# Performance work log

Measured on AMD Instinct MI355X. Metric: run time of the kernel, lower is better.

Reference implementation:

```python
import jax, jax.numpy as jnp
import numpy as np

B, C, CI, H, W = 8, 256, 128, 48, 48


def conv1x1(x, w, b):
    # x: (B,C,H,W), w: (CI,C), b: (CI,)
    return jnp.einsum('bchw,oc->bohw', x, w) + b[None, :, None, None]


def setup_inputs() -> dict:
    key = jax.random.key(0)
    ks = jax.random.split(key, 14)
    s = 1.0 / np.sqrt(C)
    d = {
        'x_1': jax.random.normal(ks[0], (B, C, H, W), jnp.float32),
        'x_2': jax.random.normal(ks[1], (B, C, H, W), jnp.float32),
    }
    names = ['v1', 'k1', 'q1', 'v2', 'k2', 'q2']
    for i, n in enumerate(names):
        d['w_' + n] = jax.random.uniform(ks[2 + 2 * i], (CI, C), jnp.float32, -s, s)
        d['b_' + n] = jax.random.uniform(ks[3 + 2 * i], (CI,), jnp.float32, -s, s)
    return d


def reference(x_1, x_2, w_v1, b_v1, w_k1, b_k1, w_q1, b_q1,
              w_v2, b_v2, w_k2, b_k2, w_q2, b_q2):
    b, ci, h, w = x_1.shape[0], w_v1.shape[0], x_1.shape[2], x_1.shape[3]
    n = h * w
    V1 = conv1x1(x_1, w_v1, b_v1).reshape(b, ci, n)
    K1 = conv1x1(x_1, w_k1, b_k1).reshape(b, ci, n)
    Q1 = conv1x1(x_1, w_q1, b_q1).reshape(b, ci, n)
    V2 = conv1x1(x_2, w_v2, b_v2).reshape(b, ci, n)
    K2 = conv1x1(x_2, w_k2, b_k2).reshape(b, ci, n)
    Q2 = conv1x1(x_2, w_q2, b_q2).reshape(b, ci, n)
    # sigmoid-gated cross attention, (B, N, N)
    R12 = jax.nn.sigmoid(jnp.einsum('bcn,bcm->bnm', Q1, K2))
    R21 = jax.nn.sigmoid(jnp.einsum('bcn,bcm->bnm', Q2, K1))
    Fu1 = jnp.einsum('bnm,bcm->bcn', R12, V2).reshape(b, ci, h, w)
    Fu2 = jnp.einsum('bnm,bcm->bcn', R21, V1).reshape(b, ci, h, w)
    y_1 = jnp.concatenate([x_1, Fu1], axis=1)
    y_2 = jnp.concatenate([x_2, Fu2], axis=1)
    return (y_1, y_2)
```

## Files before the change

### kernel.cpp

```cpp
#include <hip/hip_runtime.h>
#include <hip/hip_bf16.h>


typedef __bf16 bf16;
typedef __bf16 bf16x8 __attribute__((ext_vector_type(8)));
typedef __bf16 bf16x4 __attribute__((ext_vector_type(4)));
typedef float f32x4 __attribute__((ext_vector_type(4)));
typedef float f32x16 __attribute__((ext_vector_type(16)));
typedef unsigned int u32x4 __attribute__((ext_vector_type(4)));

#define NB 8
#define NC 256
#define NCI 128
#define NHW 2304
#define NT32 72

__global__ __launch_bounds__(256) void wconv_kernel(
    const float* __restrict__ w0, const float* __restrict__ w1,
    const float* __restrict__ w2, const float* __restrict__ w3,
    const float* __restrict__ w4, const float* __restrict__ w5,
    bf16* __restrict__ dst)
{
    int idx = (blockIdx.x * 256 + threadIdx.x) * 8;
    int m = idx >> 15;
    int off = idx & 32767;
    const float* w = (m == 0) ? w0 : (m == 1) ? w1 : (m == 2) ? w2
                   : (m == 3) ? w3 : (m == 4) ? w4 : w5;
    f32x4 a0 = *(const f32x4*)(w + off);
    f32x4 a1 = *(const f32x4*)(w + off + 4);
    bf16x8 o;
    #pragma unroll
    for (int j = 0; j < 4; ++j) { o[j] = (bf16)a0[j]; o[4 + j] = (bf16)a1[j]; }
    *(bf16x8*)(dst + idx) = o;
}

__global__ __launch_bounds__(256) void qkv_kernel(
    const float* __restrict__ x1, const float* __restrict__ x2,
    const bf16* __restrict__ wb,
    const float* __restrict__ bv1, const float* __restrict__ bk1, const float* __restrict__ bq1,
    const float* __restrict__ bv2, const float* __restrict__ bk2, const float* __restrict__ bq2,
    bf16* __restrict__ Qt, bf16* __restrict__ Kt, bf16* __restrict__ Vt,
    float* __restrict__ out)
{
    __shared__ __align__(16) bf16 Xt[32 * 264];

    int gid = blockIdx.x;
    int nt = gid % NT32;
    int s = (gid / NT32) & 1;
    int b = gid / (2 * NT32);
    int n0 = nt * 32;

    const float* x = s ? x2 : x1;
    const bf16* wv = wb + (size_t)(s * 3 + 0) * (NCI * NC);
    const bf16* wk = wb + (size_t)(s * 3 + 1) * (NCI * NC);
    const bf16* wq = wb + (size_t)(s * 3 + 2) * (NCI * NC);
    const float* bv = s ? bv2 : bv1;
    const float* bk = s ? bk2 : bk1;
    const float* bq = s ? bq2 : bq1;
    float* outy = out + (size_t)s * (NB * 384 * NHW);

    int tid = threadIdx.x;
    {
        int n_off = (tid & 3) * 8;
        int c0l = tid >> 2;
        #pragma unroll
        for (int i = 0; i < 4; ++i) {
            int c = c0l + i * 64;
            const float* src = x + ((size_t)(b * NC + c) * NHW + n0 + n_off);
            f32x4 a0 = *(const f32x4*)src;
            f32x4 a1 = *(const f32x4*)(src + 4);
            float* dsty = outy + ((size_t)(b * 384 + c) * NHW + n0 + n_off);
            *(f32x4*)dsty = a0;
            *(f32x4*)(dsty + 4) = a1;
            #pragma unroll
            for (int j = 0; j < 4; ++j) {
                Xt[(n_off + j) * 264 + c] = (bf16)a0[j];
                Xt[(n_off + 4 + j) * 264 + c] = (bf16)a1[j];
            }
        }
    }
    __syncthreads();

    int lane = tid & 63;
    int wid = tid >> 6;
    int row = lane & 15, quad = lane >> 4;
    int ci_base = wid * 32;

    f32x4 acc[3][2][2];
    #pragma unroll
    for (int t = 0; t < 3; ++t)
        #pragma unroll
        for (int mi = 0; mi < 2; ++mi)
            #pragma unroll
            for (int j = 0; j < 2; ++j)
                acc[t][mi][j] = (f32x4){0.f, 0.f, 0.f, 0.f};

    const bf16* wptr[3] = {wq, wk, wv};
    #pragma unroll
    for (int ks = 0; ks < 8; ++ks) {
        int c0 = ks * 32 + quad * 8;
        bf16x8 bfrag[2];
        #pragma unroll
        for (int j = 0; j < 2; ++j)
            bfrag[j] = *(const bf16x8*)&Xt[(j * 16 + row) * 264 + c0];
        #pragma unroll
        for (int t = 0; t < 3; ++t) {
            #pragma unroll
            for (int mi = 0; mi < 2; ++mi) {
                bf16x8 afrag = *(const bf16x8*)&wptr[t][(size_t)(ci_base + mi * 16 + row) * NC + c0];
                #pragma unroll
                for (int j = 0; j < 2; ++j)
                    acc[t][mi][j] = __builtin_amdgcn_mfma_f32_16x16x32_bf16(
                        afrag, bfrag[j], acc[t][mi][j], 0, 0, 0);
            }
        }
    }

    size_t qkbase = ((size_t)s * NB + b) * NHW * NCI;
    size_t vbase  = ((size_t)s * NB + b) * NCI * NHW;
    #pragma unroll
    for (int mi = 0; mi < 2; ++mi) {
        int ci0 = ci_base + mi * 16 + quad * 4;
        f32x4 bq4 = *(const f32x4*)&bq[ci0];
        f32x4 bk4 = *(const f32x4*)&bk[ci0];
        f32x4 bv4 = *(const f32x4*)&bv[ci0];
        #pragma unroll
        for (int j = 0; j < 2; ++j) {
            int n = n0 + j * 16 + row;
            bf16x4 pk;
            #pragma unroll
            for (int r = 0; r < 4; ++r) pk[r] = (bf16)(acc[0][mi][j][r] + bq4[r]);
            *(bf16x4*)&Qt[qkbase + (size_t)n * NCI + ci0] = pk;
            #pragma unroll
            for (int r = 0; r < 4; ++r) pk[r] = (bf16)(acc[1][mi][j][r] + bk4[r]);
            *(bf16x4*)&Kt[qkbase + (size_t)n * NCI + ci0] = pk;
            #pragma unroll
            for (int r = 0; r < 4; ++r)
                Vt[vbase + (size_t)(ci0 + r) * NHW + n] = (bf16)(acc[2][mi][j][r] + bv4[r]);
        }
    }
}

__global__ __launch_bounds__(256, 2) void attn_kernel(
    const bf16* __restrict__ Qt, const bf16* __restrict__ Kt, const bf16* __restrict__ Vt,
    float* __restrict__ out)
{
    __shared__ __align__(16) bf16 KH[2 * 64 * 128];
    __shared__ __align__(16) bf16 VH[2 * 128 * 64];

    int gid = blockIdx.x;
    int pair = (gid & 7) * 2 + ((gid >> 3) & 1);
    int nb = gid >> 4;
    int dir = pair & 1;
    int b = pair >> 1;

    int tid = threadIdx.x;
    int lane = tid & 63;
    int w = tid >> 6;
    int ns = w & 1;
    int mh = w >> 1;
    int col = lane & 31;
    int hi = lane >> 5;

    int sq = dir, skv = dir ^ 1;
    const bf16* q = Qt + ((size_t)sq  * NB + b) * (NHW * NCI);
    const bf16* k = Kt + ((size_t)skv * NB + b) * (NHW * NCI);
    const bf16* v = Vt + ((size_t)skv * NB + b) * (NCI * NHW);
    float* outy = out + (size_t)dir * (NB * 384 * NHW) + ((size_t)b * 384 + 256) * NHW;

    int kgoff[4], vgoff[4], kloff[4], vloff[4];
    #pragma unroll
    for (int i = 0; i < 4; ++i) {
        int c = tid + i * 256;
        int kr = c >> 4, kc = c & 15;
        kgoff[i] = kr * NCI + kc * 8;
        kloff[i] = kr * 128 + ((kc ^ (kr & 15)) * 8);
        int vr = c >> 3, vc = c & 7;
        vgoff[i] = vr * NHW + vc * 8;
        vloff[i] = vr * 64 + ((vc ^ (vr & 7)) * 8);
    }

    int nw = nb * 64 + ns * 32;
    bf16x8 qf[8];
    #pragma unroll
    for (int kq = 0; kq < 8; ++kq)
        qf[kq] = *(const bf16x8*)&q[(size_t)(nw + col) * NCI + kq * 16 + hi * 8];

    f32x16 o0, o1, o2, o3;
    #pragma unroll
    for (int j = 0; j < 16; ++j) { o0[j] = 0.f; o1[j] = 0.f; o2[j] = 0.f; o3[j] = 0.f; }

    bf16x8 rk[2][4], rv[2][4];
    #pragma unroll
    for (int h = 0; h < 2; ++h) {
        const bf16* kp = k + (size_t)(h * 1152) * NCI;
        const bf16* vp = v + h * 1152;
        #pragma unroll
        for (int i = 0; i < 4; ++i) {
            rk[h][i] = *(const bf16x8*)(kp + kgoff[i]);
            rv[h][i] = *(const bf16x8*)(vp + vgoff[i]);
        }
    }

    const bf16* KB = &KH[mh * (64 * 128)];
    const bf16* VB = &VH[mh * (128 * 64)];

    for (int it = 0; it < 18; ++it) {
        __syncthreads();
        #pragma unroll
        for (int h = 0; h < 2; ++h)
            #pragma unroll
            for (int i = 0; i < 4; ++i) {
                *(bf16x8*)&KH[h * (64 * 128) + kloff[i]] = rk[h][i];
                *(bf16x8*)&VH[h * (128 * 64) + vloff[i]] = rv[h][i];
            }
        __syncthreads();
        if (it < 17) {
            #pragma unroll
            for (int h = 0; h < 2; ++h) {
                const bf16* kp = k + (size_t)(h * 1152 + (it + 1) * 64) * NCI;
                const bf16* vp = v + (h * 1152 + (it + 1) * 64);
                #pragma unroll
                for (int i = 0; i < 4; ++i) {
                    rk[h][i] = *(const bf16x8*)(kp + kgoff[i]);
                    rv[h][i] = *(const bf16x8*)(vp + vgoff[i]);
                }
            }
        }

        f32x16 s0, s1;
        #pragma unroll
        for (int j = 0; j < 16; ++j) { s0[j] = 0.f; s1[j] = 0.f; }

        __builtin_amdgcn_s_setprio(1);
        #pragma unroll
        for (int kq = 0; kq < 8; ++kq) {
            bf16x8 kf0 = *(const bf16x8*)&KB[col * 128 + (((2 * kq + hi) ^ (col & 15)) * 8)];
            s0 = __builtin_amdgcn_mfma_f32_32x32x16_bf16(kf0, qf[kq], s0, 0, 0, 0);
            bf16x8 kf1 = *(const bf16x8*)&KB[(32 + col) * 128 + (((2 * kq + hi) ^ (col & 15)) * 8)];
            s1 = __builtin_amdgcn_mfma_f32_32x32x16_bf16(kf1, qf[kq], s1, 0, 0, 0);
        }
        __builtin_amdgcn_s_setprio(0);

        u32x4 pbw[4];
        #pragma unroll
        for (int ms = 0; ms < 2; ++ms) {
            float p[16];
            #pragma unroll
            for (int r = 0; r < 16; ++r) {
                float sv = (ms == 0) ? s0[r] : s1[r];
                float e = __expf(-sv);
                p[r] = __builtin_amdgcn_rcpf(1.0f + e);
            }
            #pragma unroll
            for (int kst = 0; kst < 2; ++kst) {
                unsigned int a0, a1, b0, b1;
                asm("v_cvt_pk_bf16_f32 %0, %1, %2" : "=v"(a0) : "v"(p[8*kst+0]), "v"(p[8*kst+1]));
                asm("v_cvt_pk_bf16_f32 %0, %1, %2" : "=v"(a1) : "v"(p[8*kst+2]), "v"(p[8*kst+3]));
                asm("v_cvt_pk_bf16_f32 %0, %1, %2" : "=v"(b0) : "v"(p[8*kst+4]), "v"(p[8*kst+5]));
                asm("v_cvt_pk_bf16_f32 %0, %1, %2" : "=v"(b1) : "v"(p[8*kst+6]), "v"(p[8*kst+7]));
                asm volatile("v_permlane32_swap_b32 %0, %1" : "+v"(a0), "+v"(b0));
                asm volatile("v_permlane32_swap_b32 %0, %1" : "+v"(a1), "+v"(b1));
                pbw[ms * 2 + kst] = (u32x4){a0, a1, b0, b1};
            }
        }

        __builtin_amdgcn_s_setprio(1);
        #pragma unroll
        for (int km = 0; km < 4; ++km) {
            bf16x8 pf = __builtin_bit_cast(bf16x8, pbw[km]);
            {
                bf16x8 vf = *(const bf16x8*)&VB[(0 * 32 + col) * 64 + (((2 * km + hi) ^ (col & 7)) * 8)];
                o0 = __builtin_amdgcn_mfma_f32_32x32x16_bf16(vf, pf, o0, 0, 0, 0);
            }
            {
                bf16x8 vf = *(const bf16x8*)&VB[(1 * 32 + col) * 64 + (((2 * km + hi) ^ (col & 7)) * 8)];
                o1 = __builtin_amdgcn_mfma_f32_32x32x16_bf16(vf, pf, o1, 0, 0, 0);
            }
            {
                bf16x8 vf = *(const bf16x8*)&VB[(2 * 32 + col) * 64 + (((2 * km + hi) ^ (col & 7)) * 8)];
                o2 = __builtin_amdgcn_mfma_f32_32x32x16_bf16(vf, pf, o2, 0, 0, 0);
            }
            {
                bf16x8 vf = *(const bf16x8*)&VB[(3 * 32 + col) * 64 + (((2 * km + hi) ^ (col & 7)) * 8)];
                o3 = __builtin_amdgcn_mfma_f32_32x32x16_bf16(vf, pf, o3, 0, 0, 0);
            }
        }
        __builtin_amdgcn_s_setprio(0);
    }

    float* RED = (float*)KH;

    auto red_write = [&](float* buf, const f32x16 oa, const f32x16 ob) {
        #pragma unroll
        for (int g = 0; g < 4; ++g) {
            f32x4 va, vb;
            #pragma unroll
            for (int j = 0; j < 4; ++j) { va[j] = oa[g * 4 + j]; vb[j] = ob[g * 4 + j]; }
            *(f32x4*)&buf[lane * 32 + ((g ^ (lane & 7)) * 4)] = va;
            *(f32x4*)&buf[lane * 32 + (((4 + g) ^ (lane & 7)) * 4)] = vb;
        }
    };
    auto red_fin = [&](float* buf, f32x16& oa, f32x16& ob, int ctbase) {
        #pragma unroll
        for (int g = 0; g < 4; ++g) {
            f32x4 va = *(const f32x4*)&buf[lane * 32 + ((g ^ (lane & 7)) * 4)];
            f32x4 vb = *(const f32x4*)&buf[lane * 32 + (((4 + g) ^ (lane & 7)) * 4)];
            #pragma unroll
            for (int j = 0; j < 4; ++j) { oa[g * 4 + j] += va[j]; ob[g * 4 + j] += vb[j]; }
        }
        #pragma unroll
        for (int r = 0; r < 16; ++r) {
            int cr = (r & 3) + 8 * (r >> 2) + 4 * hi;
            outy[(size_t)(ctbase * 32 + cr) * NHW + nw + col] = oa[r];
            outy[(size_t)((ctbase + 1) * 32 + cr) * NHW + nw + col] = ob[r];
        }
    };

    __syncthreads();
    if (mh == 0) red_write(RED + (ns * 2 + 0) * 2048, o2, o3);
    else         red_write(RED + (ns * 2 + 1) * 2048, o0, o1);
    __syncthreads();
    if (mh == 0) red_fin(RED + (ns * 2 + 1) * 2048, o0, o1, 0);
    else         red_fin(RED + (ns * 2 + 0) * 2048, o2, o3, 2);
}

extern "C" void kernel_launch(void* const* d_in, const int* in_sizes, int n_in,
                              void* d_out, int out_size, void* d_ws, size_t ws_size,
                              hipStream_t stream) {
    const float* x1  = (const float*)d_in[0];
    const float* x2  = (const float*)d_in[1];
    const float* wv1 = (const float*)d_in[2];  const float* bv1 = (const float*)d_in[3];
    const float* wk1 = (const float*)d_in[4];  const float* bk1 = (const float*)d_in[5];
    const float* wq1 = (const float*)d_in[6];  const float* bq1 = (const float*)d_in[7];
    const float* wv2 = (const float*)d_in[8];  const float* bv2 = (const float*)d_in[9];
    const float* wk2 = (const float*)d_in[10]; const float* bk2 = (const float*)d_in[11];
    const float* wq2 = (const float*)d_in[12]; const float* bq2 = (const float*)d_in[13];
    float* out = (float*)d_out;

    size_t per = (size_t)2 * NB * NHW * NCI;
    bf16* Qt = (bf16*)d_ws;
    bf16* Kt = Qt + per;
    bf16* Vt = Kt + per;
    bf16* wb = Vt + per;

    wconv_kernel<<<dim3(96), dim3(256), 0, stream>>>(wv1, wk1, wq1, wv2, wk2, wq2, wb);

    qkv_kernel<<<dim3(NB * 2 * NT32), dim3(256), 0, stream>>>(
        x1, x2, wb, bv1, bk1, bq1, bv2, bk2, bq2, Qt, Kt, Vt, out);

    attn_kernel<<<dim3(NB * 2 * 36), dim3(256), 0, stream>>>(Qt, Kt, Vt, out);
}
```

Baseline: 234.9 us.

## Split attention KV sequence four ways across 8 waves with LDS-resident Q

```diff
diff --git a/kernel.cpp b/kernel.cpp
--- a/kernel.cpp
+++ b/kernel.cpp
@@ -141,12 +141,14 @@
     }
 }
 
-__global__ __launch_bounds__(256, 2) void attn_kernel(
+__global__ __launch_bounds__(512, 4) void attn_kernel(
     const bf16* __restrict__ Qt, const bf16* __restrict__ Kt, const bf16* __restrict__ Vt,
     float* __restrict__ out)
 {
-    __shared__ __align__(16) bf16 KH[2 * 64 * 128];
-    __shared__ __align__(16) bf16 VH[2 * 128 * 64];
+    __shared__ __align__(16) bf16 SMEM[40960];
+    bf16* KQ = SMEM;
+    bf16* VQ = SMEM + 16384;
+    bf16* QL = SMEM + 32768;
 
     int gid = blockIdx.x;
     int pair = (gid & 7) * 2 + ((gid >> 3) & 1);
@@ -158,7 +160,7 @@
     int lane = tid & 63;
     int w = tid >> 6;
     int ns = w & 1;
-    int mh = w >> 1;
+    int mq = w >> 1;
     int col = lane & 31;
     int hi = lane >> 5;
 
@@ -168,161 +170,171 @@
     const bf16* v = Vt + ((size_t)skv * NB + b) * (NCI * NHW);
     float* outy = out + (size_t)dir * (NB * 384 * NHW) + ((size_t)b * 384 + 256) * NHW;
 
+    #pragma unroll
+    for (int i = 0; i < 2; ++i) {
+        int c = tid + i * 512;
+        int qr = c >> 4, qc = c & 15;
+        bf16x8 t = *(const bf16x8*)&q[(size_t)(nb * 64 + qr) * NCI + qc * 8];
+        *(bf16x8*)&QL[qr * 128 + ((qc ^ (qr & 15)) * 8)] = t;
+    }
+
     int kgoff[4], vgoff[4], kloff[4], vloff[4];
     #pragma unroll
     for (int i = 0; i < 4; ++i) {
-        int c = tid + i * 256;
-        int kr = c >> 4, kc = c & 15;
-        kgoff[i] = kr * NCI + kc * 8;
-        kloff[i] = kr * 128 + ((kc ^ (kr & 15)) * 8);
-        int vr = c >> 3, vc = c & 7;
-        vgoff[i] = vr * NHW + vc * 8;
-        vloff[i] = vr * 64 + ((vc ^ (vr & 7)) * 8);
+        int c = tid + i * 512;
+        int qd = c >> 9, cc = c & 511;
+        int kr = cc >> 4, kc = cc & 15;
+        kgoff[i] = (qd * 576 + kr) * NCI + kc * 8;
+        kloff[i] = qd * 4096 + kr * 128 + ((kc ^ (kr & 15)) * 8);
+        int vr = cc >> 2, vc = cc & 3;
+        vgoff[i] = vr * NHW + qd * 576 + vc * 8;
+        vloff[i] = qd * 4096 + vr * 32 + ((vc ^ ((vr >> 1) & 3)) * 8);
     }
 
     int nw = nb * 64 + ns * 32;
-    bf16x8 qf[8];
-    #pragma unroll
-    for (int kq = 0; kq < 8; ++kq)
-        qf[kq] = *(const bf16x8*)&q[(size_t)(nw + col) * NCI + kq * 16 + hi * 8];
 
     f32x16 o0, o1, o2, o3;
     #pragma unroll
     for (int j = 0; j < 16; ++j) { o0[j] = 0.f; o1[j] = 0.f; o2[j] = 0.f; o3[j] = 0.f; }
 
-    bf16x8 rk[2][4], rv[2][4];
-    #pragma unroll
-    for (int h = 0; h < 2; ++h) {
-        const bf16* kp = k + (size_t)(h * 1152) * NCI;
-        const bf16* vp = v + h * 1152;
-        #pragma unroll
-        for (int i = 0; i < 4; ++i) {
-            rk[h][i] = *(const bf16x8*)(kp + kgoff[i]);
-            rv[h][i] = *(const bf16x8*)(vp + vgoff[i]);
-        }
-    }
-
-    const bf16* KB = &KH[mh * (64 * 128)];
-    const bf16* VB = &VH[mh * (128 * 64)];
+    bf16x8 rk[4], rv[4];
+    #pragma unroll
+    for (int i = 0; i < 4; ++i) {
+        rk[i] = *(const bf16x8*)(k + kgoff[i]);
+        rv[i] = *(const bf16x8*)(v + vgoff[i]);
+    }
+
+    int krd = mq * 4096 + col * 128;
+    int qrd = (ns * 32 + col) * 128;
+    int cswz = col & 15;
+    int vsw = (col >> 1) & 3;
+    int vrd = mq * 4096 + col * 32;
 
     for (int it = 0; it < 18; ++it) {
         __syncthreads();
         #pragma unroll
-        for (int h = 0; h < 2; ++h)
+        for (int i = 0; i < 4; ++i) {
+            *(bf16x8*)&KQ[kloff[i]] = rk[i];
+            *(bf16x8*)&VQ[vloff[i]] = rv[i];
+        }
+        __syncthreads();
+
+        f32x16 s;
+        #pragma unroll
+        for (int j = 0; j < 16; ++j) s[j] = 0.f;
+
+        __builtin_amdgcn_s_setprio(1);
+        #pragma unroll
+        for (int kq = 0; kq < 8; ++kq) {
+            int ch = ((2 * kq + hi) ^ cswz) * 8;
+            bf16x8 kf = *(const bf16x8*)&KQ[krd + ch];
+            bf16x8 qf = *(const bf16x8*)&QL[qrd + ch];
+            s = __builtin_amdgcn_mfma_f32_32x32x16_bf16(kf, qf, s, 0, 0, 0);
+        }
+        __builtin_amdgcn_s_setprio(0);
+
+        if (it < 17) {
+            size_t ko = (size_t)(it + 1) * 4096;
+            int vo = (it + 1) * 32;
             #pragma unroll
             for (int i = 0; i < 4; ++i) {
-                *(bf16x8*)&KH[h * (64 * 128) + kloff[i]] = rk[h][i];
-                *(bf16x8*)&VH[h * (128 * 64) + vloff[i]] = rv[h][i];
-            }
-        __syncthreads();
-        if (it < 17) {
-            #pragma unroll
-            for (int h = 0; h < 2; ++h) {
-                const bf16* kp = k + (size_t)(h * 1152 + (it + 1) * 64) * NCI;
-                const bf16* vp = v + (h * 1152 + (it + 1) * 64);
-                #pragma unroll
-                for (int i = 0; i < 4; ++i) {
-                    rk[h][i] = *(const bf16x8*)(kp + kgoff[i]);
-                    rv[h][i] = *(const bf16x8*)(vp + vgoff[i]);
-                }
-            }
-        }
-
-        f32x16 s0, s1;
-        #pragma unroll
-        for (int j = 0; j < 16; ++j) { s0[j] = 0.f; s1[j] = 0.f; }
+                rk[i] = *(const bf16x8*)(k + ko + kgoff[i]);
+                rv[i] = *(const bf16x8*)(v + vo + vgoff[i]);
+            }
+        }
+
+        float p[16];
+        #pragma unroll
+        for (int r = 0; r < 16; ++r) {
+            float e = __expf(-s[r]);
+            p[r] = __builtin_amdgcn_rcpf(1.0f + e);
+        }
+        u32x4 pbw[2];
+        #pragma unroll
+        for (int kst = 0; kst < 2; ++kst) {
+            unsigned int a0, a1, b0, b1;
+            asm("v_cvt_pk_bf16_f32 %0, %1, %2" : "=v"(a0) : "v"(p[8*kst+0]), "v"(p[8*kst+1]));
+            asm("v_cvt_pk_bf16_f32 %0, %1, %2" : "=v"(a1) : "v"(p[8*kst+2]), "v"(p[8*kst+3]));
+            asm("v_cvt_pk_bf16_f32 %0, %1, %2" : "=v"(b0) : "v"(p[8*kst+4]), "v"(p[8*kst+5]));
+            asm("v_cvt_pk_bf16_f32 %0, %1, %2" : "=v"(b1) : "v"(p[8*kst+6]), "v"(p[8*kst+7]));
+            asm volatile("v_permlane32_swap_b32 %0, %1" : "+v"(a0), "+v"(b0));
+            asm volatile("v_permlane32_swap_b32 %0, %1" : "+v"(a1), "+v"(b1));
+            pbw[kst] = (u32x4){a0, a1, b0, b1};
+        }
 
         __builtin_amdgcn_s_setprio(1);
         #pragma unroll
-        for (int kq = 0; kq < 8; ++kq) {
-            bf16x8 kf0 = *(const bf16x8*)&KB[col * 128 + (((2 * kq + hi) ^ (col & 15)) * 8)];
-            s0 = __builtin_amdgcn_mfma_f32_32x32x16_bf16(kf0, qf[kq], s0, 0, 0, 0);
-            bf16x8 kf1 = *(const bf16x8*)&KB[(32 + col) * 128 + (((2 * kq + hi) ^ (col & 15)) * 8)];
-            s1 = __builtin_amdgcn_mfma_f32_32x32x16_bf16(kf1, qf[kq], s1, 0, 0, 0);
+        for (int km = 0; km < 2; ++km) {
+            bf16x8 pf = __builtin_bit_cast(bf16x8, pbw[km]);
+            int mch = ((2 * km + hi) ^ vsw) * 8;
+            {
+                bf16x8 vf = *(const bf16x8*)&VQ[vrd + 0 * 1024 + mch];
+                o0 = __builtin_amdgcn_mfma_f32_32x32x16_bf16(vf, pf, o0, 0, 0, 0);
+            }
+            {
+                bf16x8 vf = *(const bf16x8*)&VQ[vrd + 1 * 1024 + mch];
+                o1 = __builtin_amdgcn_mfma_f32_32x32x16_bf16(vf, pf, o1, 0, 0, 0);
+            }
+            {
+                bf16x8 vf = *(const bf16x8*)&VQ[vrd + 2 * 1024 + mch];
+                o2 = __builtin_amdgcn_mfma_f32_32x32x16_bf16(vf, pf, o2, 0, 0, 0);
+            }
+            {
+                bf16x8 vf = *(const bf16x8*)&VQ[vrd + 3 * 1024 + mch];
+                o3 = __builtin_amdgcn_mfma_f32_32x32x16_bf16(vf, pf, o3, 0, 0, 0);
+            }
         }
         __builtin_amdgcn_s_setprio(0);
-
-        u32x4 pbw[4];
-        #pragma unroll
-        for (int ms = 0; ms < 2; ++ms) {
-            float p[16];
-            #pragma unroll
-            for (int r = 0; r < 16; ++r) {
-                float sv = (ms == 0) ? s0[r] : s1[r];
-                float e = __expf(-sv);
-                p[r] = __builtin_amdgcn_rcpf(1.0f + e);
-            }
-            #pragma unroll
-            for (int kst = 0; kst < 2; ++kst) {
-                unsigned int a0, a1, b0, b1;
-                asm("v_cvt_pk_bf16_f32 %0, %1, %2" : "=v"(a0) : "v"(p[8*kst+0]), "v"(p[8*kst+1]));
-                asm("v_cvt_pk_bf16_f32 %0, %1, %2" : "=v"(a1) : "v"(p[8*kst+2]), "v"(p[8*kst+3]));
-                asm("v_cvt_pk_bf16_f32 %0, %1, %2" : "=v"(b0) : "v"(p[8*kst+4]), "v"(p[8*kst+5]));
-                asm("v_cvt_pk_bf16_f32 %0, %1, %2" : "=v"(b1) : "v"(p[8*kst+6]), "v"(p[8*kst+7]));
-                asm volatile("v_permlane32_swap_b32 %0, %1" : "+v"(a0), "+v"(b0));
-                asm volatile("v_permlane32_swap_b32 %0, %1" : "+v"(a1), "+v"(b1));
-                pbw[ms * 2 + kst] = (u32x4){a0, a1, b0, b1};
-            }
-        }
-
-        __builtin_amdgcn_s_setprio(1);
-        #pragma unroll
-        for (int km = 0; km < 4; ++km) {
-            bf16x8 pf = __builtin_bit_cast(bf16x8, pbw[km]);
-            {
-                bf16x8 vf = *(const bf16x8*)&VB[(0 * 32 + col) * 64 + (((2 * km + hi) ^ (col & 7)) * 8)];
-                o0 = __builtin_amdgcn_mfma_f32_32x32x16_bf16(vf, pf, o0, 0, 0, 0);
-            }
-            {
-                bf16x8 vf = *(const bf16x8*)&VB[(1 * 32 + col) * 64 + (((2 * km + hi) ^ (col & 7)) * 8)];
-                o1 = __builtin_amdgcn_mfma_f32_32x32x16_bf16(vf, pf, o1, 0, 0, 0);
-            }
-            {
-                bf16x8 vf = *(const bf16x8*)&VB[(2 * 32 + col) * 64 + (((2 * km + hi) ^ (col & 7)) * 8)];
-                o2 = __builtin_amdgcn_mfma_f32_32x32x16_bf16(vf, pf, o2, 0, 0, 0);
-            }
-            {
-                bf16x8 vf = *(const bf16x8*)&VB[(3 * 32 + col) * 64 + (((2 * km + hi) ^ (col & 7)) * 8)];
-                o3 = __builtin_amdgcn_mfma_f32_32x32x16_bf16(vf, pf, o3, 0, 0, 0);
-            }
-        }
-        __builtin_amdgcn_s_setprio(0);
-    }
-
-    float* RED = (float*)KH;
-
-    auto red_write = [&](float* buf, const f32x16 oa, const f32x16 ob) {
+    }
+
+    float* RED = (float*)SMEM;
+
+    auto wpart = [&](float* buf, const f32x16& a, int cb) {
         #pragma unroll
         for (int g = 0; g < 4; ++g) {
-            f32x4 va, vb;
-            #pragma unroll
-            for (int j = 0; j < 4; ++j) { va[j] = oa[g * 4 + j]; vb[j] = ob[g * 4 + j]; }
-            *(f32x4*)&buf[lane * 32 + ((g ^ (lane & 7)) * 4)] = va;
-            *(f32x4*)&buf[lane * 32 + (((4 + g) ^ (lane & 7)) * 4)] = vb;
+            f32x4 v4;
+            #pragma unroll
+            for (int j = 0; j < 4; ++j) v4[j] = a[g * 4 + j];
+            *(f32x4*)&buf[lane * 64 + (((cb * 4 + g) ^ (lane & 15)) * 4)] = v4;
         }
     };
-    auto red_fin = [&](float* buf, f32x16& oa, f32x16& ob, int ctbase) {
+    auto rpart = [&](float* buf, f32x16& a, int cb) {
         #pragma unroll
         for (int g = 0; g < 4; ++g) {
-            f32x4 va = *(const f32x4*)&buf[lane * 32 + ((g ^ (lane & 7)) * 4)];
-            f32x4 vb = *(const f32x4*)&buf[lane * 32 + (((4 + g) ^ (lane & 7)) * 4)];
-            #pragma unroll
-            for (int j = 0; j < 4; ++j) { oa[g * 4 + j] += va[j]; ob[g * 4 + j] += vb[j]; }
-        }
+            f32x4 v4 = *(const f32x4*)&buf[lane * 64 + (((cb * 4 + g) ^ (lane & 15)) * 4)];
+            #pragma unroll
+            for (int j = 0; j < 4; ++j) a[g * 4 + j] += v4[j];
+        }
+    };
+
+    __syncthreads();
+    if (mq >= 2) {
+        float* buf = RED + (ns * 2 + (mq & 1)) * 4096;
+        wpart(buf, o0, 0); wpart(buf, o1, 1); wpart(buf, o2, 2); wpart(buf, o3, 3);
+    }
+    __syncthreads();
+    if (mq < 2) {
+        float* buf = RED + (ns * 2 + mq) * 4096;
+        rpart(buf, o0, 0); rpart(buf, o1, 1); rpart(buf, o2, 2); rpart(buf, o3, 3);
+    }
+    __syncthreads();
+    if (mq == 1) {
+        float* buf = RED + ns * 4096;
+        wpart(buf, o0, 0); wpart(buf, o1, 1); wpart(buf, o2, 2); wpart(buf, o3, 3);
+    }
+    __syncthreads();
+    if (mq == 0) {
+        float* buf = RED + ns * 4096;
+        rpart(buf, o0, 0); rpart(buf, o1, 1); rpart(buf, o2, 2); rpart(buf, o3, 3);
         #pragma unroll
         for (int r = 0; r < 16; ++r) {
             int cr = (r & 3) + 8 * (r >> 2) + 4 * hi;
-            outy[(size_t)(ctbase * 32 + cr) * NHW + nw + col] = oa[r];
-            outy[(size_t)((ctbase + 1) * 32 + cr) * NHW + nw + col] = ob[r];
-        }
-    };
-
-    __syncthreads();
-    if (mh == 0) red_write(RED + (ns * 2 + 0) * 2048, o2, o3);
-    else         red_write(RED + (ns * 2 + 1) * 2048, o0, o1);
-    __syncthreads();
-    if (mh == 0) red_fin(RED + (ns * 2 + 1) * 2048, o0, o1, 0);
-    else         red_fin(RED + (ns * 2 + 0) * 2048, o2, o3, 2);
+            outy[(size_t)(0 * 32 + cr) * NHW + nw + col] = o0[r];
+            outy[(size_t)(1 * 32 + cr) * NHW + nw + col] = o1[r];
+            outy[(size_t)(2 * 32 + cr) * NHW + nw + col] = o2[r];
+            outy[(size_t)(3 * 32 + cr) * NHW + nw + col] = o3[r];
+        }
+    }
 }
 
 extern "C" void kernel_launch(void* const* d_in, const int* in_sizes, int n_in,
@@ -349,5 +361,5 @@
     qkv_kernel<<<dim3(NB * 2 * NT32), dim3(256), 0, stream>>>(
         x1, x2, wb, bv1, bk1, bq1, bv2, bk2, bq2, Qt, Kt, Vt, out);
 
-    attn_kernel<<<dim3(NB * 2 * 36), dim3(256), 0, stream>>>(Qt, Kt, Vt, out);
+    attn_kernel<<<dim3(NB * 2 * 36), dim3(512), 0, stream>>>(Qt, Kt, Vt, out);
 }
```

Result: slower. 457.3 us (+94.7%).
